# Performance work log

Measured on AMD Instinct MI355X. Metric: run time of the kernel, lower is better.

## Reference

```python
import jax, jax.numpy as jnp
import numpy as np

K = 4          # kNN neighbors (includes self, distance 0)
NUM_CONVS = 3


def _mlp(h, Ws, bs):
    # Linear -> ELU repeated, final Linear has no activation (matches nn.Sequential)
    for i, (W, b) in enumerate(zip(Ws, bs)):
        h = h @ W + b
        if i < len(Ws) - 1:
            h = jax.nn.elu(h)
    return h


def _gravnet(emb, Ws, bs, Wh, bh, Wo1, Wo2, bo2):
    # PyG GravNetConv: project to learned space s and features h, kNN in s,
    # edge weight exp(-10*d^2), mean+max aggregate, out = lin_out1(x) + lin_out2(agg)
    s = emb @ Ws + bs                        # [B,N,S]
    h = emb @ Wh + bh                        # [B,N,P]
    sq = jnp.sum(s * s, axis=-1)             # [B,N]
    d2 = sq[:, :, None] + sq[:, None, :] - 2.0 * jnp.einsum('bns,bms->bnm', s, s)
    negd2, idx = jax.lax.top_k(-d2, K)       # [B,N,K] nearest (incl. self)
    w = jnp.exp(-10.0 * jnp.maximum(-negd2, 0.0))   # clamp tiny negative d2 from numerics
    neigh = jax.vmap(lambda hb, ib: hb[ib])(h, idx)  # [B,N,K,P]
    msg = neigh * w[..., None]
    agg = jnp.concatenate([msg.mean(axis=2), msg.max(axis=2)], axis=-1)  # [B,N,2P]
    return emb @ Wo1 + agg @ Wo2 + bo2


def setup_inputs() -> dict:
    key = jax.random.key(0)
    keys = iter(jax.random.split(key, 128))

    def lin(kin, kout, bias=True):
        lim = 1.0 / np.sqrt(kin)
        W = jax.random.uniform(next(keys), (kin, kout), minval=-lim, maxval=lim, dtype=jnp.float32)
        if not bias:
            return W
        b = jax.random.uniform(next(keys), (kout,), minval=-lim, maxval=lim, dtype=jnp.float32)
        return W, b

    d = {"x": jax.random.normal(next(keys), (8, 4096, 12), dtype=jnp.float32)}
    for name, dims in [("nn1", [12, 126, 126, 126, 32]),
                       ("nn2", [44, 256, 256, 256, 6]),
                       ("nn3", [18, 256, 256, 256, 6])]:
        for i in range(4):
            W, b = lin(dims[i], dims[i + 1])
            d[f"{name}_w{i}"] = W
            d[f"{name}_b{i}"] = b
    E, S, P = 32, 4, 8
    ws, bss, wh, bhs, wo1, wo2, bo2 = [], [], [], [], [], [], []
    for _ in range(NUM_CONVS):
        W, b = lin(E, S); ws.append(W); bss.append(b)
        W, b = lin(E, P); wh.append(W); bhs.append(b)
        wo1.append(lin(E, E, bias=False))
        W, b = lin(2 * P, E); wo2.append(W); bo2.append(b)
    d["conv_ws"] = jnp.stack(ws);  d["conv_bs"] = jnp.stack(bss)
    d["conv_wh"] = jnp.stack(wh);  d["conv_bh"] = jnp.stack(bhs)
    d["conv_wo1"] = jnp.stack(wo1)
    d["conv_wo2"] = jnp.stack(wo2); d["conv_bo2"] = jnp.stack(bo2)
    return d


def reference(x,
              nn1_w0, nn1_b0, nn1_w1, nn1_b1, nn1_w2, nn1_b2, nn1_w3, nn1_b3,
              nn2_w0, nn2_b0, nn2_w1, nn2_b1, nn2_w2, nn2_b2, nn2_w3, nn2_b3,
              nn3_w0, nn3_b0, nn3_w1, nn3_b1, nn3_w2, nn3_b2, nn3_w3, nn3_b3,
              conv_ws, conv_bs, conv_wh, conv_bh, conv_wo1, conv_wo2, conv_bo2):
    emb = _mlp(x, [nn1_w0, nn1_w1, nn1_w2, nn1_w3], [nn1_b0, nn1_b1, nn1_b2, nn1_b3])
    for i in range(NUM_CONVS):
        emb = _gravnet(emb, conv_ws[i], conv_bs[i], conv_wh[i], conv_bh[i],
                       conv_wo1[i], conv_wo2[i], conv_bo2[i])
    preds_id = _mlp(jnp.concatenate([x, emb], axis=-1),
                    [nn2_w0, nn2_w1, nn2_w2, nn2_w3], [nn2_b0, nn2_b1, nn2_b2, nn2_b3])
    preds_p4 = _mlp(jnp.concatenate([x, preds_id], axis=-1),
                    [nn3_w0, nn3_w1, nn3_w2, nn3_w3], [nn3_b0, nn3_b1, nn3_b2, nn3_b3])
    return jnp.concatenate([preds_id, preds_p4], axis=-1)  # [B,N,12]
```

## Files before the change

### kernel.cpp

```cpp
#include <hip/hip_runtime.h>
#include <hip/hip_bf16.h>
#include <cfloat>
#include <climits>

#define NN_TOTAL 32768
#define NPTS     4096

typedef __attribute__((ext_vector_type(8))) short short8;
typedef __attribute__((ext_vector_type(4))) float f32x4;

__device__ __forceinline__ void split_bf16(float v, unsigned short& h, unsigned short& l)
{
    __hip_bfloat16 hb = __float2bfloat16(v);
    float hf = __bfloat162float(hb);
    __hip_bfloat16 lb = __float2bfloat16(v - hf);
    h = __builtin_bit_cast(unsigned short, hb);
    l = __builtin_bit_cast(unsigned short, lb);
}

__device__ __forceinline__ float elu_fast(float v)
{
    return (v > 0.f) ? v : (__expf(v) - 1.f);
}

__device__ __forceinline__ void gload16(const unsigned short* g, unsigned short* l)
{
    __builtin_amdgcn_global_load_lds(
        (const __attribute__((address_space(1))) unsigned int*)g,
        (__attribute__((address_space(3))) unsigned int*)l, 16, 0, 0);
}

struct PrepArgs {
    const float* W[12];
    int K[12];
    int N[12];
    int ksh[12];
    int off[12];
    int blk0[12];
};

__global__ __launch_bounds__(256) void prep_all(
    PrepArgs a, unsigned short* __restrict__ th, unsigned short* __restrict__ tl)
{
    int l = 0;
    #pragma unroll
    for (int j = 1; j < 12; ++j) l += (blockIdx.x >= (unsigned)a.blk0[j]) ? 1 : 0;
    const int le = (blockIdx.x - a.blk0[l]) * 256 + threadIdx.x;
    const int ksh = a.ksh[l];
    const int n = le >> ksh;
    const int k = le & ((1 << ksh) - 1);
    const float v = (n < a.N[l] && k < a.K[l]) ? a.W[l][(size_t)k * a.N[l] + n] : 0.f;
    unsigned short h, lo;
    split_bf16(v, h, lo);
    th[a.off[l] + le] = h;
    tl[a.off[l] + le] = lo;
}

__global__ __launch_bounds__(256) void pack_x64(
    const float* __restrict__ x, unsigned short* __restrict__ Xh, unsigned short* __restrict__ Xl)
{
    const int gid = blockIdx.x * 256 + threadIdx.x;
    const int r = gid >> 3, c8 = (gid & 7) * 8;
    unsigned short h[8], l[8];
    #pragma unroll
    for (int j = 0; j < 8; ++j) {
        const int col = c8 + j;
        const float v = (col < 12) ? x[(size_t)r * 12 + col] : 0.f;
        split_bf16(v, h[j], l[j]);
    }
    *(int4*)(Xh + (size_t)r * 64 + c8) = *(int4*)h;
    *(int4*)(Xl + (size_t)r * 64 + c8) = *(int4*)l;
}

__global__ __launch_bounds__(256) void cat2_pack(
    const float* __restrict__ x, const float* __restrict__ emb,
    unsigned short* __restrict__ Xh, unsigned short* __restrict__ Xl)
{
    const int gid = blockIdx.x * 256 + threadIdx.x;
    const int r = gid >> 3, c8 = (gid & 7) * 8;
    unsigned short h[8], l[8];
    #pragma unroll
    for (int j = 0; j < 8; ++j) {
        const int col = c8 + j;
        float v = 0.f;
        if (col < 12)      v = x[(size_t)r * 12 + col];
        else if (col < 44) v = emb[(size_t)r * 32 + (col - 12)];
        split_bf16(v, h[j], l[j]);
    }
    *(int4*)(Xh + (size_t)r * 64 + c8) = *(int4*)h;
    *(int4*)(Xl + (size_t)r * 64 + c8) = *(int4*)l;
}

__global__ __launch_bounds__(256) void cat3_pack(
    const float* __restrict__ x, const float* __restrict__ dout,
    unsigned short* __restrict__ Xh, unsigned short* __restrict__ Xl)
{
    const int gid = blockIdx.x * 256 + threadIdx.x;
    const int r = gid >> 3, c8 = (gid & 7) * 8;
    unsigned short h[8], l[8];
    #pragma unroll
    for (int j = 0; j < 8; ++j) {
        const int col = c8 + j;
        float v = 0.f;
        if (col < 12)      v = x[(size_t)r * 12 + col];
        else if (col < 18) v = dout[(size_t)r * 12 + (col - 12)];
        split_bf16(v, h[j], l[j]);
    }
    *(int4*)(Xh + (size_t)r * 64 + c8) = *(int4*)h;
    *(int4*)(Xl + (size_t)r * 64 + c8) = *(int4*)l;
}

template<int NF>
__global__ __launch_bounds__(256, 2) void gemm_mfma3(
    const unsigned short* __restrict__ Ah, const unsigned short* __restrict__ Al,
    const unsigned short* __restrict__ Bh, const unsigned short* __restrict__ Bl,
    const float* __restrict__ bias, int Kp, int N, int act,
    float* __restrict__ Cf, int ldcf,
    unsigned short* __restrict__ Ch, unsigned short* __restrict__ Cl, int ldcb, int padN)
{
    __shared__ unsigned short ldsbuf[2 * 128 * 64 + 2 * NF * 32 * 64];
    unsigned short* ldsAh = ldsbuf;
    unsigned short* ldsAl = ldsbuf + 128 * 64;
    unsigned short* ldsBh = ldsbuf + 2 * 128 * 64;
    unsigned short* ldsBl = ldsbuf + 2 * 128 * 64 + NF * 32 * 64;

    const int tid  = threadIdx.x;
    const int wave = tid >> 6, lane = tid & 63;
    const int wr = wave >> 1, wc = wave & 1;
    const int row0 = blockIdx.x * 128;
    const int col0 = blockIdx.y * (NF * 32);
    const int r16 = lane & 15, kg = lane >> 4;

    f32x4 acc[4][NF];
    #pragma unroll
    for (int m = 0; m < 4; ++m)
        #pragma unroll
        for (int n = 0; n < NF; ++n)
            #pragma unroll
            for (int r = 0; r < 4; ++r) acc[m][n][r] = 0.f;

    for (int k0 = 0; k0 < Kp; k0 += 64) {
        __syncthreads();
        #pragma unroll
        for (int c = tid; c < 1024; c += 256) {
            const int r  = c >> 3;
            const int kc = ((c & 7) ^ (r & 7)) * 8;
            const size_t go = (size_t)(row0 + r) * Kp + k0 + kc;
            gload16(Ah + go, ldsAh + c * 8);
            gload16(Al + go, ldsAl + c * 8);
        }
        #pragma unroll
        for (int c = tid; c < NF * 256; c += 256) {
            const int r  = c >> 3;
            const int kc = ((c & 7) ^ (r & 7)) * 8;
            const size_t go = (size_t)(col0 + r) * Kp + k0 + kc;
            gload16(Bh + go, ldsBh + c * 8);
            gload16(Bl + go, ldsBl + c * 8);
        }
        __syncthreads();

        #pragma unroll
        for (int kk = 0; kk < 2; ++kk) {
            const int lc = kk * 4 + kg;
            short8 ah[4], al[4], bh[NF], bl[NF];
            #pragma unroll
            for (int m = 0; m < 4; ++m) {
                const int rr = wr * 64 + m * 16 + r16;
                const int off = rr * 64 + ((lc ^ (rr & 7)) * 8);
                ah[m] = *(const short8*)&ldsAh[off];
                al[m] = *(const short8*)&ldsAl[off];
            }
            #pragma unroll
            for (int n = 0; n < NF; ++n) {
                const int br = (NF == 4 ? wc * 64 + n * 16 : wc * 16) + r16;
                const int off = br * 64 + ((lc ^ (br & 7)) * 8);
                bh[n] = *(const short8*)&ldsBh[off];
                bl[n] = *(const short8*)&ldsBl[off];
            }
            #pragma unroll
            for (int m = 0; m < 4; ++m)
                #pragma unroll
                for (int n = 0; n < NF; ++n) {
                    acc[m][n] = __builtin_amdgcn_mfma_f32_16x16x32_bf16(ah[m], bh[n], acc[m][n], 0, 0, 0);
                    acc[m][n] = __builtin_amdgcn_mfma_f32_16x16x32_bf16(ah[m], bl[n], acc[m][n], 0, 0, 0);
                    acc[m][n] = __builtin_amdgcn_mfma_f32_16x16x32_bf16(al[m], bh[n], acc[m][n], 0, 0, 0);
                }
        }
    }

    #pragma unroll
    for (int m = 0; m < 4; ++m) {
        #pragma unroll
        for (int n = 0; n < NF; ++n) {
            const int col = col0 + (NF == 4 ? wc * 64 + n * 16 : wc * 16) + r16;
            #pragma unroll
            for (int r = 0; r < 4; ++r) {
                const int row = row0 + wr * 64 + m * 16 + kg * 4 + r;
                if (col < N) {
                    float v = acc[m][n][r] + bias[col];
                    if (act) v = elu_fast(v);
                    if (Cf) {
                        Cf[(size_t)row * ldcf + col] = v;
                    } else {
                        unsigned short h, l;
                        split_bf16(v, h, l);
                        Ch[(size_t)row * ldcb + col] = h;
                        Cl[(size_t)row * ldcb + col] = l;
                    }
                } else if (Ch && col < padN) {
                    Ch[(size_t)row * ldcb + col] = 0;
                    Cl[(size_t)row * ldcb + col] = 0;
                }
            }
        }
    }
}

__global__ __launch_bounds__(64) void conv_proj(
    const float* __restrict__ emb, const float* __restrict__ Ws,
    const float* __restrict__ bs, const float* __restrict__ Wh,
    const float* __restrict__ bh,
    float* __restrict__ s_out, float* __restrict__ sq_out, float* __restrict__ h_out)
{
    __shared__ float ws_s[32 * 4];
    __shared__ float wh_s[32 * 8];
    __shared__ float bs_s[4];
    __shared__ float bh_s[8];
    const int tid = threadIdx.x;
    for (int i = tid; i < 128; i += 64) ws_s[i] = Ws[i];
    for (int i = tid; i < 256; i += 64) wh_s[i] = Wh[i];
    if (tid < 4) bs_s[tid] = bs[tid];
    if (tid >= 8 && tid < 16) bh_s[tid - 8] = bh[tid - 8];
    __syncthreads();

    const int row = blockIdx.x * 64 + tid;
    float e[32];
    #pragma unroll
    for (int i = 0; i < 8; i++)
        *(float4*)&e[i * 4] = *(const float4*)(emb + (size_t)row * 32 + i * 4);

    float sv[4];
    #pragma unroll
    for (int c = 0; c < 4; c++) {
        float a = e[0] * ws_s[c];
        #pragma unroll
        for (int k = 1; k < 32; k++) a = fmaf(e[k], ws_s[k * 4 + c], a);
        sv[c] = a + bs_s[c];
    }
    float sq = sv[0] * sv[0];
    sq = fmaf(sv[1], sv[1], sq);
    sq = fmaf(sv[2], sv[2], sq);
    sq = fmaf(sv[3], sv[3], sq);

    float hv[8];
    #pragma unroll
    for (int c = 0; c < 8; c++) {
        float a = e[0] * wh_s[c];
        #pragma unroll
        for (int k = 1; k < 32; k++) a = fmaf(e[k], wh_s[k * 8 + c], a);
        hv[c] = a + bh_s[c];
    }

    *(float4*)(s_out + (size_t)row * 4) = *(float4*)&sv[0];
    sq_out[row] = sq;
    *(float4*)(h_out + (size_t)row * 8)     = *(float4*)&hv[0];
    *(float4*)(h_out + (size_t)row * 8 + 4) = *(float4*)&hv[4];
}

__device__ __forceinline__ void merge44(const float* ad, const int* ai,
                                        const float* bd, const int* bi,
                                        float* od, int* oi)
{
    int a = 0, b = 0;
    #pragma unroll
    for (int k = 0; k < 4; ++k) {
        bool ta;
        if (a < 4 && b < 4)
            ta = (ad[a] < bd[b]) || (ad[a] == bd[b] && ai[a] < bi[b]);
        else
            ta = (a < 4);
        if (ta) { od[k] = ad[a]; oi[k] = ai[a]; ++a; }
        else    { od[k] = bd[b]; oi[k] = bi[b]; ++b; }
    }
}

__global__ __launch_bounds__(256) void knn_top4_part(
    const float* __restrict__ s, const float* __restrict__ sq,
    float* __restrict__ pd, int* __restrict__ pi)
{
    __shared__ float4 cs[256];
    __shared__ float  csq[256];

    const int tid  = threadIdx.x;
    const int pg   = blockIdx.x >> 4;
    const int sp   = blockIdx.x & 15;
    const int p0   = pg << 8;
    const int base = (p0 >> 12) << 12;
    const int row  = p0 + tid;

    const float4 sn  = *(const float4*)(s + (size_t)row * 4);
    const float  sqn = sq[row];

    const int m0 = sp << 8;
    {
        const int gm = base + m0 + tid;
        cs[tid]  = *(const float4*)(s + (size_t)gm * 4);
        csq[tid] = sq[gm];
    }
    __syncthreads();

    float bd[4] = {FLT_MAX, FLT_MAX, FLT_MAX, FLT_MAX};
    int   bi[4] = {INT_MAX, INT_MAX, INT_MAX, INT_MAX};

    #pragma unroll 8
    for (int i = 0; i < 256; ++i) {
        const float4 cm = cs[i];
        const float  cq = csq[i];
        float dot = sn.x * cm.x;
        dot = fmaf(sn.y, cm.y, dot);
        dot = fmaf(sn.z, cm.z, dot);
        dot = fmaf(sn.w, cm.w, dot);
        const float d2 = (sqn + cq) - 2.f * dot;
        const int m = m0 + i;
        const bool c3 = d2 < bd[3];
        const bool c2 = d2 < bd[2];
        const bool c1 = d2 < bd[1];
        const bool c0 = d2 < bd[0];
        bi[3] = c3 ? (c2 ? bi[2] : m) : bi[3];
        bi[2] = c2 ? (c1 ? bi[1] : m) : bi[2];
        bi[1] = c1 ? (c0 ? bi[0] : m) : bi[1];
        bi[0] = c0 ? m : bi[0];
        bd[3] = __builtin_amdgcn_fmed3f(bd[2], bd[3], d2);
        bd[2] = __builtin_amdgcn_fmed3f(bd[1], bd[2], d2);
        bd[1] = __builtin_amdgcn_fmed3f(bd[0], bd[1], d2);
        bd[0] = fminf(bd[0], d2);
    }

    const size_t o = (((size_t)pg * 16 + sp) * 256 + tid) * 4;
    *(float4*)(pd + o) = *(float4*)&bd[0];
    *(int4*)(pi + o)   = *(int4*)&bi[0];
}

__global__ __launch_bounds__(64) void conv_agg(
    const float* __restrict__ emb, const float* __restrict__ h,
    const float* __restrict__ pd, const int* __restrict__ pi,
    const float* __restrict__ Wo1, const float* __restrict__ Wo2,
    const float* __restrict__ bo2, float* __restrict__ out,
    const float* __restrict__ Ws2, const float* __restrict__ bs2,
    const float* __restrict__ Wh2, const float* __restrict__ bh2,
    float* __restrict__ s_out, float* __restrict__ sq_out, float* __restrict__ h_out)
{
    __shared__ float w1[1024];
    __shared__ float w2[512];
    __shared__ float b2[32];
    __shared__ float ws_s[128];
    __shared__ float wh_s[256];
    __shared__ float bs_s[4];
    __shared__ float bh_s[8];
    const int tid = threadIdx.x;
    for (int i = tid; i < 1024; i += 64) w1[i] = Wo1[i];
    for (int i = tid; i < 512;  i += 64) w2[i] = Wo2[i];
    if (tid < 32) b2[tid] = bo2[tid];
    if (Ws2) {
        for (int i = tid; i < 128; i += 64) ws_s[i] = Ws2[i];
        for (int i = tid; i < 256; i += 64) wh_s[i] = Wh2[i];
        if (tid < 4) bs_s[tid] = bs2[tid];
        if (tid >= 8 && tid < 16) bh_s[tid - 8] = bh2[tid - 8];
    }
    __syncthreads();

    const int row  = blockIdx.x * 64 + tid;
    const int pg   = row >> 8;
    const int ln   = row & 255;
    const int base = (row >> 12) << 12;

    float ad[4];
    int   ai[4];
    {
        const size_t o = ((size_t)pg * 16 * 256 + ln) * 4;
        *(float4*)&ad[0] = *(const float4*)(pd + o);
        *(int4*)&ai[0]   = *(const int4*)(pi + o);
    }
    #pragma unroll
    for (int sp = 1; sp < 16; ++sp) {
        const size_t o = (((size_t)pg * 16 + sp) * 256 + ln) * 4;
        float bdv[4], od[4];
        int   biv[4], oi[4];
        *(float4*)&bdv[0] = *(const float4*)(pd + o);
        *(int4*)&biv[0]   = *(const int4*)(pi + o);
        merge44(ad, ai, bdv, biv, od, oi);
        #pragma unroll
        for (int k = 0; k < 4; ++k) { ad[k] = od[k]; ai[k] = oi[k]; }
    }

    float e[32];
    #pragma unroll
    for (int i = 0; i < 8; i++)
        *(float4*)&e[i * 4] = *(const float4*)(emb + (size_t)row * 32 + i * 4);

    float msum[8], mmax[8];
    #pragma unroll
    for (int dd = 0; dd < 8; dd++) { msum[dd] = 0.f; mmax[dd] = -FLT_MAX; }

    #pragma unroll
    for (int k = 0; k < 4; k++) {
        const int g    = base + ai[k];
        const float wk = __expf(-10.f * fmaxf(ad[k], 0.f));
        float hv[8];
        *(float4*)&hv[0] = *(const float4*)(h + (size_t)g * 8);
        *(float4*)&hv[4] = *(const float4*)(h + (size_t)g * 8 + 4);
        #pragma unroll
        for (int dd = 0; dd < 8; dd++) {
            const float m = hv[dd] * wk;
            msum[dd] += m;
            mmax[dd] = fmaxf(mmax[dd], m);
        }
    }

    float agg[16];
    #pragma unroll
    for (int dd = 0; dd < 8; dd++) { agg[dd] = msum[dd] * 0.25f; agg[8 + dd] = mmax[dd]; }

    float o32[32];
    #pragma unroll
    for (int j = 0; j < 32; j++) {
        float a = e[0] * w1[j];
        #pragma unroll
        for (int k = 1; k < 32; k++) a = fmaf(e[k], w1[k * 32 + j], a);
        float g = agg[0] * w2[j];
        #pragma unroll
        for (int k = 1; k < 16; k++) g = fmaf(agg[k], w2[k * 32 + j], g);
        o32[j] = a + g + b2[j];
        out[(size_t)row * 32 + j] = o32[j];
    }

    if (Ws2) {
        float sv[4];
        #pragma unroll
        for (int c = 0; c < 4; c++) {
            float a = o32[0] * ws_s[c];
            #pragma unroll
            for (int k = 1; k < 32; k++) a = fmaf(o32[k], ws_s[k * 4 + c], a);
            sv[c] = a + bs_s[c];
        }
        float sq2 = sv[0] * sv[0];
        sq2 = fmaf(sv[1], sv[1], sq2);
        sq2 = fmaf(sv[2], sv[2], sq2);
        sq2 = fmaf(sv[3], sv[3], sq2);

        float hv[8];
        #pragma unroll
        for (int c = 0; c < 8; c++) {
            float a = o32[0] * wh_s[c];
            #pragma unroll
            for (int k = 1; k < 32; k++) a = fmaf(o32[k], wh_s[k * 8 + c], a);
            hv[c] = a + bh_s[c];
        }
        *(float4*)(s_out + (size_t)row * 4) = *(float4*)&sv[0];
        sq_out[row] = sq2;
        *(float4*)(h_out + (size_t)row * 8)     = *(float4*)&hv[0];
        *(float4*)(h_out + (size_t)row * 8 + 4) = *(float4*)&hv[4];
    }
}

extern "C" void kernel_launch(void* const* d_in, const int* in_sizes, int n_in,
                              void* d_out, int out_size, void* d_ws, size_t ws_size,
                              hipStream_t stream)
{
    const float* x = (const float*)d_in[0];
    const float* nn1_w[4] = {(const float*)d_in[1], (const float*)d_in[3], (const float*)d_in[5], (const float*)d_in[7]};
    const float* nn1_b[4] = {(const float*)d_in[2], (const float*)d_in[4], (const float*)d_in[6], (const float*)d_in[8]};
    const float* nn2_w[4] = {(const float*)d_in[9],  (const float*)d_in[11], (const float*)d_in[13], (const float*)d_in[15]};
    const float* nn2_b[4] = {(const float*)d_in[10], (const float*)d_in[12], (const float*)d_in[14], (const float*)d_in[16]};
    const float* nn3_w[4] = {(const float*)d_in[17], (const float*)d_in[19], (const float*)d_in[21], (const float*)d_in[23]};
    const float* nn3_b[4] = {(const float*)d_in[18], (const float*)d_in[20], (const float*)d_in[22], (const float*)d_in[24]};
    const float* conv_ws  = (const float*)d_in[25];
    const float* conv_bs  = (const float*)d_in[26];
    const float* conv_wh  = (const float*)d_in[27];
    const float* conv_bh  = (const float*)d_in[28];
    const float* conv_wo1 = (const float*)d_in[29];
    const float* conv_wo2 = (const float*)d_in[30];
    const float* conv_bo2 = (const float*)d_in[31];

    float* outp = (float*)d_out;
    const int M = NN_TOTAL;

    char* p = (char*)d_ws;
    auto take = [&](size_t bytes) { char* r = p; p += (bytes + 255) & ~size_t(255); return r; };
    unsigned short* Xa_h = (unsigned short*)take((size_t)M * 256 * 2);
    unsigned short* Xa_l = (unsigned short*)take((size_t)M * 256 * 2);
    unsigned short* Xb_h = (unsigned short*)take((size_t)M * 256 * 2);
    unsigned short* Xb_l = (unsigned short*)take((size_t)M * 256 * 2);
    float* embA = (float*)take((size_t)M * 32 * 4);
    float* embB = (float*)take((size_t)M * 32 * 4);
    unsigned short* WH = (unsigned short*)take((size_t)450000 * 2);
    unsigned short* WL = (unsigned short*)take((size_t)450000 * 2);

    char* q = (char*)Xa_h;
    auto takeq = [&](size_t bytes) { char* r = q; q += (bytes + 255) & ~size_t(255); return r; };
    float* sbuf  = (float*)takeq((size_t)M * 4 * 4);
    float* sqb   = (float*)takeq((size_t)M * 4);
    float* hbufA = (float*)takeq((size_t)M * 8 * 4);
    float* hbufB = (float*)takeq((size_t)M * 8 * 4);
    float* pdb   = (float*)takeq((size_t)M * 16 * 4 * 4);
    int*   pib   = (int*)takeq((size_t)M * 16 * 4 * 4);

    struct LW { int K, N, Kp, Np, off; };
    LW lw[12];
    const float* Ws_[12] = {nn1_w[0], nn1_w[1], nn1_w[2], nn1_w[3],
                            nn2_w[0], nn2_w[1], nn2_w[2], nn2_w[3],
                            nn3_w[0], nn3_w[1], nn3_w[2], nn3_w[3]};
    const int Ks_[12] = {12, 126, 126, 126,  44, 256, 256, 256,  18, 256, 256, 256};
    const int Ns_[12] = {126, 126, 126, 32,  256, 256, 256, 6,   256, 256, 256, 6};
    PrepArgs pa;
    int off = 0, blk = 0;
    for (int i = 0; i < 12; ++i) {
        lw[i].K = Ks_[i]; lw[i].N = Ns_[i];
        lw[i].Kp = (Ks_[i] + 63) & ~63;
        lw[i].Np = (Ns_[i] <= 32) ? 32 : ((Ns_[i] + 127) & ~127);
        lw[i].off = off;
        pa.W[i] = Ws_[i];
        pa.K[i] = Ks_[i]; pa.N[i] = Ns_[i];
        pa.ksh[i] = __builtin_ctz(lw[i].Kp);
        pa.off[i] = off;
        pa.blk0[i] = blk;
        off += lw[i].Kp * lw[i].Np;
        blk += lw[i].Kp * lw[i].Np / 256;
    }
    prep_all<<<blk, 256, 0, stream>>>(pa, WH, WL);

    auto mfma = [&](const unsigned short* Ah, const unsigned short* Al, int li,
                    const float* bias, int act,
                    float* Cf, int ldcf,
                    unsigned short* Chh, unsigned short* Cll, int ldcb, int padN, int nf) {
        if (nf == 4) {
            dim3 g(M / 128, lw[li].Np / 128);
            gemm_mfma3<4><<<g, 256, 0, stream>>>(Ah, Al, WH + lw[li].off, WL + lw[li].off,
                                                 bias, lw[li].Kp, lw[li].N, act,
                                                 Cf, ldcf, Chh, Cll, ldcb, padN);
        } else {
            dim3 g(M / 128, 1);
            gemm_mfma3<1><<<g, 256, 0, stream>>>(Ah, Al, WH + lw[li].off, WL + lw[li].off,
                                                 bias, lw[li].Kp, lw[li].N, act,
                                                 Cf, ldcf, Chh, Cll, ldcb, padN);
        }
    };

    pack_x64<<<M * 8 / 256, 256, 0, stream>>>(x, Xa_h, Xa_l);
    mfma(Xa_h, Xa_l, 0, nn1_b[0], 1, nullptr, 0, Xb_h, Xb_l, 128, 128, 4);
    mfma(Xb_h, Xb_l, 1, nn1_b[1], 1, nullptr, 0, Xa_h, Xa_l, 128, 128, 4);
    mfma(Xa_h, Xa_l, 2, nn1_b[2], 1, nullptr, 0, Xb_h, Xb_l, 128, 128, 4);
    mfma(Xb_h, Xb_l, 3, nn1_b[3], 0, embA, 32, nullptr, nullptr, 0, 0, 1);

    conv_proj<<<M / 64, 64, 0, stream>>>(
        embA, conv_ws, conv_bs, conv_wh, conv_bh, sbuf, sqb, hbufA);
    float* ecur = embA;  float* enext = embB;
    float* hcur = hbufA; float* hnext = hbufB;
    for (int i = 0; i < 3; i++) {
        knn_top4_part<<<(M / 256) * 16, 256, 0, stream>>>(sbuf, sqb, pdb, pib);
        const bool fuse = (i < 2);
        conv_agg<<<M / 64, 64, 0, stream>>>(
            ecur, hcur, pdb, pib,
            conv_wo1 + i * 1024, conv_wo2 + i * 512, conv_bo2 + i * 32, enext,
            fuse ? conv_ws + (i + 1) * 128 : nullptr,
            fuse ? conv_bs + (i + 1) * 4   : nullptr,
            fuse ? conv_wh + (i + 1) * 256 : nullptr,
            fuse ? conv_bh + (i + 1) * 8   : nullptr,
            sbuf, sqb, hnext);
        float* t = ecur; ecur = enext; enext = t;
        t = hcur; hcur = hnext; hnext = t;
    }

    cat2_pack<<<M * 8 / 256, 256, 0, stream>>>(x, ecur, Xa_h, Xa_l);
    mfma(Xa_h, Xa_l, 4, nn2_b[0], 1, nullptr, 0, Xb_h, Xb_l, 256, 256, 4);
    mfma(Xb_h, Xb_l, 5, nn2_b[1], 1, nullptr, 0, Xa_h, Xa_l, 256, 256, 4);
    mfma(Xa_h, Xa_l, 6, nn2_b[2], 1, nullptr, 0, Xb_h, Xb_l, 256, 256, 4);
    mfma(Xb_h, Xb_l, 7, nn2_b[3], 0, outp, 12, nullptr, nullptr, 0, 0, 1);

    cat3_pack<<<M * 8 / 256, 256, 0, stream>>>(x, outp, Xa_h, Xa_l);
    mfma(Xa_h, Xa_l, 8, nn3_b[0], 1, nullptr, 0, Xb_h, Xb_l, 256, 256, 4);
    mfma(Xb_h, Xb_l, 9, nn3_b[1], 1, nullptr, 0, Xa_h, Xa_l, 256, 256, 4);
    mfma(Xa_h, Xa_l, 10, nn3_b[2], 1, nullptr, 0, Xb_h, Xb_l, 256, 256, 4);
    mfma(Xb_h, Xb_l, 11, nn3_b[3], 0, outp + 6, 12, nullptr, nullptr, 0, 0, 1);
}
```

Before: 581.4 us.

## Stage GEMM epilogue through LDS and fuse concat-pack kernels into producers

The GEMM epilogue now writes accumulators to shared memory, then has each thread handle a contiguous half-row, so output stores become vectorized float4 and int4 writes instead of scattered scalar stores. The separate cat2_pack and cat3_pack kernels are removed. The last conv_agg and the nn2 final GEMM now write the split bf16 concatenated inputs for the next MLP directly, reusing the emb buffers as scratch. This cuts two kernel launches, an intermediate round trip through global memory, and uncoalesced epilogue writes. The cost is an extra LDS pass with two barriers per GEMM, plus scalar short stores in the fused pack paths.

```diff
diff --git a/kernel.cpp b/kernel.cpp
--- a/kernel.cpp
+++ b/kernel.cpp
@@ -72,53 +72,20 @@
     *(int4*)(Xl + (size_t)r * 64 + c8) = *(int4*)l;
 }
 
-__global__ __launch_bounds__(256) void cat2_pack(
-    const float* __restrict__ x, const float* __restrict__ emb,
-    unsigned short* __restrict__ Xh, unsigned short* __restrict__ Xl)
-{
-    const int gid = blockIdx.x * 256 + threadIdx.x;
-    const int r = gid >> 3, c8 = (gid & 7) * 8;
-    unsigned short h[8], l[8];
-    #pragma unroll
-    for (int j = 0; j < 8; ++j) {
-        const int col = c8 + j;
-        float v = 0.f;
-        if (col < 12)      v = x[(size_t)r * 12 + col];
-        else if (col < 44) v = emb[(size_t)r * 32 + (col - 12)];
-        split_bf16(v, h[j], l[j]);
-    }
-    *(int4*)(Xh + (size_t)r * 64 + c8) = *(int4*)h;
-    *(int4*)(Xl + (size_t)r * 64 + c8) = *(int4*)l;
-}
-
-__global__ __launch_bounds__(256) void cat3_pack(
-    const float* __restrict__ x, const float* __restrict__ dout,
-    unsigned short* __restrict__ Xh, unsigned short* __restrict__ Xl)
-{
-    const int gid = blockIdx.x * 256 + threadIdx.x;
-    const int r = gid >> 3, c8 = (gid & 7) * 8;
-    unsigned short h[8], l[8];
-    #pragma unroll
-    for (int j = 0; j < 8; ++j) {
-        const int col = c8 + j;
-        float v = 0.f;
-        if (col < 12)      v = x[(size_t)r * 12 + col];
-        else if (col < 18) v = dout[(size_t)r * 12 + (col - 12)];
-        split_bf16(v, h[j], l[j]);
-    }
-    *(int4*)(Xh + (size_t)r * 64 + c8) = *(int4*)h;
-    *(int4*)(Xl + (size_t)r * 64 + c8) = *(int4*)l;
-}
-
 template<int NF>
 __global__ __launch_bounds__(256, 2) void gemm_mfma3(
     const unsigned short* __restrict__ Ah, const unsigned short* __restrict__ Al,
     const unsigned short* __restrict__ Bh, const unsigned short* __restrict__ Bl,
     const float* __restrict__ bias, int Kp, int N, int act,
     float* __restrict__ Cf, int ldcf,
-    unsigned short* __restrict__ Ch, unsigned short* __restrict__ Cl, int ldcb, int padN)
-{
-    __shared__ unsigned short ldsbuf[2 * 128 * 64 + 2 * NF * 32 * 64];
+    unsigned short* __restrict__ Ch, unsigned short* __restrict__ Cl, int ldcb,
+    unsigned short* __restrict__ Eh, unsigned short* __restrict__ El,
+    const float* __restrict__ xsrc)
+{
+    constexpr int ES  = NF * 32 + 4;
+    constexpr int STG = 2 * 128 * 64 + 2 * NF * 32 * 64;
+    constexpr int EPI = 128 * ES * 2;
+    __shared__ unsigned short ldsbuf[(STG > EPI) ? STG : EPI];
     unsigned short* ldsAh = ldsbuf;
     unsigned short* ldsAl = ldsbuf + 128 * 64;
     unsigned short* ldsBh = ldsbuf + 2 * 128 * 64;
@@ -188,29 +155,82 @@
         }
     }
 
-    #pragma unroll
-    for (int m = 0; m < 4; ++m) {
+    __syncthreads();
+    float* eb = (float*)ldsbuf;
+    #pragma unroll
+    for (int m = 0; m < 4; ++m)
         #pragma unroll
         for (int n = 0; n < NF; ++n) {
-            const int col = col0 + (NF == 4 ? wc * 64 + n * 16 : wc * 16) + r16;
+            const int ec = (NF == 4 ? wc * 64 + n * 16 : wc * 16) + r16;
             #pragma unroll
             for (int r = 0; r < 4; ++r) {
-                const int row = row0 + wr * 64 + m * 16 + kg * 4 + r;
-                if (col < N) {
-                    float v = acc[m][n][r] + bias[col];
-                    if (act) v = elu_fast(v);
-                    if (Cf) {
-                        Cf[(size_t)row * ldcf + col] = v;
-                    } else {
-                        unsigned short h, l;
-                        split_bf16(v, h, l);
-                        Ch[(size_t)row * ldcb + col] = h;
-                        Cl[(size_t)row * ldcb + col] = l;
-                    }
-                } else if (Ch && col < padN) {
-                    Ch[(size_t)row * ldcb + col] = 0;
-                    Cl[(size_t)row * ldcb + col] = 0;
-                }
+                const int er = wr * 64 + m * 16 + kg * 4 + r;
+                eb[er * ES + ec] = acc[m][n][r];
+            }
+        }
+    __syncthreads();
+
+    constexpr int CPT = NF * 16;
+    const int rr = tid >> 1, hh = tid & 1;
+    const int c0 = hh * CPT;
+    const int grow = row0 + rr;
+
+    float vals[CPT];
+    #pragma unroll
+    for (int j = 0; j < CPT; j += 4)
+        *(float4*)&vals[j] = *(float4*)&eb[rr * ES + c0 + j];
+
+    #pragma unroll
+    for (int j = 0; j < CPT; ++j) {
+        const int col = col0 + c0 + j;
+        float v = 0.f;
+        if (col < N) {
+            v = vals[j] + bias[col];
+            if (act) v = elu_fast(v);
+        }
+        vals[j] = v;
+    }
+
+    if (Cf) {
+        if (col0 + c0 + CPT <= N) {
+            #pragma unroll
+            for (int j = 0; j < CPT; j += 4)
+                *(float4*)(Cf + (size_t)grow * ldcf + col0 + c0 + j) = *(float4*)&vals[j];
+        } else {
+            #pragma unroll
+            for (int j = 0; j < CPT; ++j) {
+                const int col = col0 + c0 + j;
+                if (col < N) Cf[(size_t)grow * ldcf + col] = vals[j];
+            }
+        }
+    }
+    if (Ch) {
+        #pragma unroll
+        for (int jc = 0; jc < CPT / 8; ++jc) {
+            unsigned short h8[8], l8[8];
+            #pragma unroll
+            for (int e = 0; e < 8; ++e) split_bf16(vals[jc * 8 + e], h8[e], l8[e]);
+            *(int4*)(Ch + (size_t)grow * ldcb + col0 + c0 + jc * 8) = *(int4*)h8;
+            *(int4*)(Cl + (size_t)grow * ldcb + col0 + c0 + jc * 8) = *(int4*)l8;
+        }
+    }
+    if (Eh) {
+        if (hh == 0) {
+            #pragma unroll
+            for (int j = 0; j < 12; ++j) {
+                unsigned short h2, l2;
+                split_bf16(xsrc[(size_t)grow * 12 + j], h2, l2);
+                Eh[(size_t)grow * 64 + j] = h2; El[(size_t)grow * 64 + j] = l2;
+            }
+            #pragma unroll
+            for (int j = 0; j < 6; ++j) {
+                unsigned short h2, l2;
+                split_bf16(vals[j], h2, l2);
+                Eh[(size_t)grow * 64 + 12 + j] = h2; El[(size_t)grow * 64 + 12 + j] = l2;
+            }
+        } else {
+            for (int j = 18; j < 64; ++j) {
+                Eh[(size_t)grow * 64 + j] = 0; El[(size_t)grow * 64 + j] = 0;
             }
         }
     }
@@ -348,7 +368,9 @@
     const float* __restrict__ bo2, float* __restrict__ out,
     const float* __restrict__ Ws2, const float* __restrict__ bs2,
     const float* __restrict__ Wh2, const float* __restrict__ bh2,
-    float* __restrict__ s_out, float* __restrict__ sq_out, float* __restrict__ h_out)
+    float* __restrict__ s_out, float* __restrict__ sq_out, float* __restrict__ h_out,
+    unsigned short* __restrict__ Exh, unsigned short* __restrict__ Exl,
+    const float* __restrict__ xsrc)
 {
     __shared__ float w1[1024];
     __shared__ float w2[512];
@@ -431,7 +453,28 @@
         #pragma unroll
         for (int k = 1; k < 16; k++) g = fmaf(agg[k], w2[k * 32 + j], g);
         o32[j] = a + g + b2[j];
-        out[(size_t)row * 32 + j] = o32[j];
+    }
+
+    if (Exh) {
+        #pragma unroll
+        for (int j = 0; j < 12; ++j) {
+            unsigned short h2, l2;
+            split_bf16(xsrc[(size_t)row * 12 + j], h2, l2);
+            Exh[(size_t)row * 64 + j] = h2; Exl[(size_t)row * 64 + j] = l2;
+        }
+        #pragma unroll
+        for (int j = 0; j < 32; ++j) {
+            unsigned short h2, l2;
+            split_bf16(o32[j], h2, l2);
+            Exh[(size_t)row * 64 + 12 + j] = h2; Exl[(size_t)row * 64 + 12 + j] = l2;
+        }
+        #pragma unroll
+        for (int j = 44; j < 64; ++j) {
+            Exh[(size_t)row * 64 + j] = 0; Exl[(size_t)row * 64 + j] = 0;
+        }
+    } else {
+        #pragma unroll
+        for (int j = 0; j < 32; j++) out[(size_t)row * 32 + j] = o32[j];
     }
 
     if (Ws2) {
@@ -504,6 +547,10 @@
     float* hbufB = (float*)takeq((size_t)M * 8 * 4);
     float* pdb   = (float*)takeq((size_t)M * 16 * 4 * 4);
     int*   pib   = (int*)takeq((size_t)M * 16 * 4 * 4);
+    unsigned short* XC_h = (unsigned short*)embB;
+    unsigned short* XC_l = (unsigned short*)takeq((size_t)M * 64 * 2);
+    unsigned short* XD_h = (unsigned short*)embA;
+    unsigned short* XD_l = (unsigned short*)embB;
 
     struct LW { int K, N, Kp, Np, off; };
     LW lw[12];
@@ -532,25 +579,27 @@
     auto mfma = [&](const unsigned short* Ah, const unsigned short* Al, int li,
                     const float* bias, int act,
                     float* Cf, int ldcf,
-                    unsigned short* Chh, unsigned short* Cll, int ldcb, int padN, int nf) {
+                    unsigned short* Chh, unsigned short* Cll, int ldcb, int nf,
+                    unsigned short* Eh = nullptr, unsigned short* El = nullptr,
+                    const float* xs = nullptr) {
         if (nf == 4) {
             dim3 g(M / 128, lw[li].Np / 128);
             gemm_mfma3<4><<<g, 256, 0, stream>>>(Ah, Al, WH + lw[li].off, WL + lw[li].off,
                                                  bias, lw[li].Kp, lw[li].N, act,
-                                                 Cf, ldcf, Chh, Cll, ldcb, padN);
+                                                 Cf, ldcf, Chh, Cll, ldcb, Eh, El, xs);
         } else {
             dim3 g(M / 128, 1);
             gemm_mfma3<1><<<g, 256, 0, stream>>>(Ah, Al, WH + lw[li].off, WL + lw[li].off,
                                                  bias, lw[li].Kp, lw[li].N, act,
-                                                 Cf, ldcf, Chh, Cll, ldcb, padN);
+                                                 Cf, ldcf, Chh, Cll, ldcb, Eh, El, xs);
         }
     };
 
     pack_x64<<<M * 8 / 256, 256, 0, stream>>>(x, Xa_h, Xa_l);
-    mfma(Xa_h, Xa_l, 0, nn1_b[0], 1, nullptr, 0, Xb_h, Xb_l, 128, 128, 4);
-    mfma(Xb_h, Xb_l, 1, nn1_b[1], 1, nullptr, 0, Xa_h, Xa_l, 128, 128, 4);
-    mfma(Xa_h, Xa_l, 2, nn1_b[2], 1, nullptr, 0, Xb_h, Xb_l, 128, 128, 4);
-    mfma(Xb_h, Xb_l, 3, nn1_b[3], 0, embA, 32, nullptr, nullptr, 0, 0, 1);
+    mfma(Xa_h, Xa_l, 0, nn1_b[0], 1, nullptr, 0, Xb_h, Xb_l, 128, 4);
+    mfma(Xb_h, Xb_l, 1, nn1_b[1], 1, nullptr, 0, Xa_h, Xa_l, 128, 4);
+    mfma(Xa_h, Xa_l, 2, nn1_b[2], 1, nullptr, 0, Xb_h, Xb_l, 128, 4);
+    mfma(Xb_h, Xb_l, 3, nn1_b[3], 0, embA, 32, nullptr, nullptr, 0, 1);
 
     conv_proj<<<M / 64, 64, 0, stream>>>(
         embA, conv_ws, conv_bs, conv_wh, conv_bh, sbuf, sqb, hbufA);
@@ -559,27 +608,28 @@
     for (int i = 0; i < 3; i++) {
         knn_top4_part<<<(M / 256) * 16, 256, 0, stream>>>(sbuf, sqb, pdb, pib);
         const bool fuse = (i < 2);
+        const bool last = (i == 2);
         conv_agg<<<M / 64, 64, 0, stream>>>(
             ecur, hcur, pdb, pib,
-            conv_wo1 + i * 1024, conv_wo2 + i * 512, conv_bo2 + i * 32, enext,
+            conv_wo1 + i * 1024, conv_wo2 + i * 512, conv_bo2 + i * 32,
+            last ? nullptr : enext,
             fuse ? conv_ws + (i + 1) * 128 : nullptr,
             fuse ? conv_bs + (i + 1) * 4   : nullptr,
             fuse ? conv_wh + (i + 1) * 256 : nullptr,
             fuse ? conv_bh + (i + 1) * 8   : nullptr,
-            sbuf, sqb, hnext);
+            sbuf, sqb, hnext,
+            last ? XC_h : nullptr, last ? XC_l : nullptr, last ? x : nullptr);
         float* t = ecur; ecur = enext; enext = t;
         t = hcur; hcur = hnext; hnext = t;
     }
 
-    cat2_pack<<<M * 8 / 256, 256, 0, stream>>>(x, ecur, Xa_h, Xa_l);
-    mfma(Xa_h, Xa_l, 4, nn2_b[0], 1, nullptr, 0, Xb_h, Xb_l, 256, 256, 4);
-    mfma(Xb_h, Xb_l, 5, nn2_b[1], 1, nullptr, 0, Xa_h, Xa_l, 256, 256, 4);
-    mfma(Xa_h, Xa_l, 6, nn2_b[2], 1, nullptr, 0, Xb_h, Xb_l, 256, 256, 4);
-    mfma(Xb_h, Xb_l, 7, nn2_b[3], 0, outp, 12, nullptr, nullptr, 0, 0, 1);
-
-    cat3_pack<<<M * 8 / 256, 256, 0, stream>>>(x, outp, Xa_h, Xa_l);
-    mfma(Xa_h, Xa_l, 8, nn3_b[0], 1, nullptr, 0, Xb_h, Xb_l, 256, 256, 4);
-    mfma(Xb_h, Xb_l, 9, nn3_b[1], 1, nullptr, 0, Xa_h, Xa_l, 256, 256, 4);
-    mfma(Xa_h, Xa_l, 10, nn3_b[2], 1, nullptr, 0, Xb_h, Xb_l, 256, 256, 4);
-    mfma(Xb_h, Xb_l, 11, nn3_b[3], 0, outp + 6, 12, nullptr, nullptr, 0, 0, 1);
-}
+    mfma(XC_h, XC_l, 4, nn2_b[0], 1, nullptr, 0, Xb_h, Xb_l, 256, 4);
+    mfma(Xb_h, Xb_l, 5, nn2_b[1], 1, nullptr, 0, Xa_h, Xa_l, 256, 4);
+    mfma(Xa_h, Xa_l, 6, nn2_b[2], 1, nullptr, 0, Xb_h, Xb_l, 256, 4);
+    mfma(Xb_h, Xb_l, 7, nn2_b[3], 0, outp, 12, nullptr, nullptr, 0, 1, XD_h, XD_l, x);
+
+    mfma(XD_h, XD_l, 8, nn3_b[0], 1, nullptr, 0, Xb_h, Xb_l, 256, 4);
+    mfma(Xb_h, Xb_l, 9, nn3_b[1], 1, nullptr, 0, Xa_h, Xa_l, 256, 4);
+    mfma(Xa_h, Xa_l, 10, nn3_b[2], 1, nullptr, 0, Xb_h, Xb_l, 256, 4);
+    mfma(Xb_h, Xb_l, 11, nn3_b[3], 0, outp + 6, 12, nullptr, nullptr, 0, 1);
+}
```

After: 599.5 us. +3.1%, slower.
